# Optimization experiments

Measured on AMD Instinct MI355X. Metric: run time of the kernel, lower is better.

The kernel has to match this reference:

```python
import jax, jax.numpy as jnp
import numpy as np

NEG_SLOPE = 0.2
EPS = 1e-16  # matches PyG softmax epsilon


def gat_conv(x, src, dst, W, att_src, att_dst, bias):
    """PyG-style GATConv (concat heads, self-loops already in src/dst).
    x: [N, F_in]; W: [F_in, H*C]; att_*: [H, C]; bias: [H*C]."""
    N = x.shape[0]
    H, C = att_src.shape
    h = (x @ W).reshape(N, H, C)                       # [N,H,C]
    a_src = jnp.einsum('nhc,hc->nh', h, att_src)       # [N,H]
    a_dst = jnp.einsum('nhc,hc->nh', h, att_dst)
    e = jax.nn.leaky_relu(a_src[src] + a_dst[dst], NEG_SLOPE)   # [E,H]
    # segment softmax over incoming edges of each dst node
    e_max = jax.ops.segment_max(e, dst, num_segments=N)         # [N,H]
    e_max = jnp.where(jnp.isfinite(e_max), e_max, 0.0)
    e_exp = jnp.exp(e - e_max[dst])                              # [E,H]
    denom = jax.ops.segment_sum(e_exp, dst, num_segments=N)     # [N,H]
    alpha = e_exp / (denom[dst] + EPS)                           # [E,H]
    msg = h[src] * alpha[:, :, None]                             # [E,H,C]
    out = jax.ops.segment_sum(msg, dst, num_segments=N)         # [N,H,C]
    return out.reshape(N, H * C) + bias


def setup_inputs() -> dict:
    key = jax.random.key(0)
    ks = jax.random.split(key, 16)
    N, E = 50000, 800000
    F_in, C, H = 1280, 32, 8
    HC = H * C
    NG = 64  # graphs in batch
    x = jax.random.normal(ks[0], (N, F_in), dtype=jnp.float32)
    edge_index = jax.random.randint(ks[1], (2, E), 0, N, dtype=jnp.int64)
    batch = jnp.sort(jax.random.randint(ks[2], (N,), 0, NG, dtype=jnp.int64))
    s = 1.0 / np.sqrt(F_in)
    W1 = jax.random.normal(ks[3], (F_in, HC), dtype=jnp.float32) * s
    as1 = jax.random.normal(ks[4], (H, C), dtype=jnp.float32) * 0.1
    ad1 = jax.random.normal(ks[5], (H, C), dtype=jnp.float32) * 0.1
    b1 = jnp.zeros((HC,), dtype=jnp.float32)
    s2 = 1.0 / np.sqrt(HC)
    W2 = jax.random.normal(ks[6], (HC, HC), dtype=jnp.float32) * s2
    as2 = jax.random.normal(ks[7], (H, C), dtype=jnp.float32) * 0.1
    ad2 = jax.random.normal(ks[8], (H, C), dtype=jnp.float32) * 0.1
    b2 = jnp.zeros((HC,), dtype=jnp.float32)
    lin1_w = jax.random.normal(ks[9], (HC, 128), dtype=jnp.float32) * s2
    lin1_b = jnp.zeros((128,), dtype=jnp.float32)
    lin2_w = jax.random.normal(ks[10], (128, 1), dtype=jnp.float32) * (1.0 / np.sqrt(128))
    lin2_b = jnp.zeros((1,), dtype=jnp.float32)
    return {"x": x, "edge_index": edge_index, "batch": batch,
            "W1": W1, "as1": as1, "ad1": ad1, "b1": b1,
            "W2": W2, "as2": as2, "ad2": ad2, "b2": b2,
            "lin1_w": lin1_w, "lin1_b": lin1_b, "lin2_w": lin2_w, "lin2_b": lin2_b}


def reference(x, edge_index, batch, W1, as1, ad1, b1, W2, as2, ad2, b2,
              lin1_w, lin1_b, lin2_w, lin2_b):
    N = x.shape[0]
    NG = 64
    loops = jnp.arange(N, dtype=edge_index.dtype)
    src = jnp.concatenate([edge_index[0], loops])  # add self-loops (PyG default)
    dst = jnp.concatenate([edge_index[1], loops])
    h = jax.nn.relu(gat_conv(x, src, dst, W1, as1, ad1, b1))
    h = jax.nn.relu(gat_conv(h, src, dst, W2, as2, ad2, b2))
    # global mean pool over graphs
    sums = jax.ops.segment_sum(h, batch, num_segments=NG)               # [NG,HC]
    cnts = jax.ops.segment_sum(jnp.ones((N, 1), h.dtype), batch, num_segments=NG)
    pooled = sums / jnp.maximum(cnts, 1.0)
    z = jax.nn.relu(pooled @ lin1_w + lin1_b)
    out = z @ lin2_w + lin2_b                                            # [NG,1]
    return out.squeeze(-1)
```

## Files before the change

kernel.cpp:

```cpp
#include <hip/hip_runtime.h>
#include <hip/hip_bf16.h>
#include <math.h>

#define HC 256
#define NH 8
#define NEG_SLOPE 0.2f
#define CHW 64
#define LDA 136
#define MR 32

typedef unsigned short u16;
typedef __attribute__((ext_vector_type(8))) short bf16x8;
typedef __attribute__((ext_vector_type(4))) float f32x4;

__device__ __forceinline__ u16 f2bf(float f) {
    unsigned int u = __float_as_uint(f);
    u += 0x7FFFu + ((u >> 16) & 1u);
    return (u16)(u >> 16);
}
__device__ __forceinline__ float bf2f(u16 s) {
    return __uint_as_float(((unsigned int)s) << 16);
}
__device__ __forceinline__ f32x4 bf4f(ushort4 v) {
    f32x4 r;
    r[0] = bf2f(v.x); r[1] = bf2f(v.y); r[2] = bf2f(v.z); r[3] = bf2f(v.w);
    return r;
}

#define BAR_LDS()                                                  \
    do {                                                           \
        asm volatile("s_waitcnt lgkmcnt(0)" ::: "memory");         \
        __builtin_amdgcn_s_barrier();                              \
        __builtin_amdgcn_sched_barrier(0);                         \
    } while (0)

__global__ __launch_bounds__(256) void pack_b_split(const float* __restrict__ B, int K,
                                                    u16* __restrict__ Bh,
                                                    u16* __restrict__ Bl) {
    const int g = blockIdx.x * 256 + threadIdx.x;
    const int lane = g & 63;
    const int f = (g >> 6) & 15;
    const int kt = g >> 10;
    const int col = f * 16 + (lane & 15);
    const int k0 = kt * 32 + (lane >> 4) * 8;
    bf16x8 hv, lv;
#pragma unroll
    for (int e = 0; e < 8; e++) {
        const float v = B[(size_t)(k0 + e) * HC + col];
        const u16 h = f2bf(v);
        hv[e] = (short)h;
        lv[e] = (short)f2bf(v - bf2f(h));
    }
    const size_t off = (size_t)g * 8;
    *(bf16x8*)(Bh + off) = hv;
    *(bf16x8*)(Bl + off) = lv;
}

__global__ __launch_bounds__(256) void gemm_fused_split(
    const float* __restrict__ A,
    const u16* __restrict__ Bh, const u16* __restrict__ Bl,
    float* __restrict__ C, int M, int K) {
    __shared__ u16 ldsA[2][MR * LDA];
    const int tid = threadIdx.x;
    const int wid = tid >> 6;
    const int lane = tid & 63;
    const int rowblk = blockIdx.x;
    const int NG4 = K >> 7;
    const int rot = rowblk % NG4;

    f32x4 acc[2][4];
#pragma unroll
    for (int i = 0; i < 2; i++)
#pragma unroll
        for (int j = 0; j < 4; j++) acc[i][j] = (f32x4)0.f;

    const int srow = tid >> 3;
    const int scc = (tid & 7) * 16;
    const int grow = rowblk * MR + srow;
    const float* aptr = (grow < M) ? (A + (size_t)grow * K + scc) : nullptr;
    const int woff = srow * LDA + scc;

    float4 pf[4];
    auto loadAg = [&](int gg) {
#pragma unroll
        for (int q = 0; q < 4; q++) {
            pf[q] = make_float4(0.f, 0.f, 0.f, 0.f);
            if (aptr) pf[q] = *(const float4*)(aptr + gg * 128 + q * 4);
        }
    };
    auto stageg = [&](int buf) {
#pragma unroll
        for (int p = 0; p < 2; p++) {
            const float vv[8] = {pf[2 * p].x,     pf[2 * p].y,
                                 pf[2 * p].z,     pf[2 * p].w,
                                 pf[2 * p + 1].x, pf[2 * p + 1].y,
                                 pf[2 * p + 1].z, pf[2 * p + 1].w};
            bf16x8 hv;
#pragma unroll
            for (int e = 0; e < 8; e++) hv[e] = (short)f2bf(vv[e]);
            *(bf16x8*)&ldsA[buf][woff + p * 8] = hv;
        }
    };
    auto readA = [&](int buf, int kk, bf16x8* ah) {
#pragma unroll
        for (int i = 0; i < 2; i++)
            ah[i] = *(const bf16x8*)&ldsA[buf][(i * 16 + (lane & 15)) * LDA +
                                              kk * 32 + (lane >> 4) * 8];
    };
    auto loadB = [&](int kt, bf16x8* bh, bf16x8* bl) {
        const u16* bHp = Bh + ((size_t)kt * 16 + wid * 4) * 512 + lane * 8;
        const u16* bLp = Bl + ((size_t)kt * 16 + wid * 4) * 512 + lane * 8;
#pragma unroll
        for (int j = 0; j < 4; j++) {
            bh[j] = *(const bf16x8*)(bHp + j * 512);
            bl[j] = *(const bf16x8*)(bLp + j * 512);
        }
    };
    auto mfma_tile = [&](const bf16x8* ah, const bf16x8* bh, const bf16x8* bl) {
#pragma unroll
        for (int i = 0; i < 2; i++)
#pragma unroll
            for (int j = 0; j < 4; j++) {
                acc[i][j] = __builtin_amdgcn_mfma_f32_16x16x32_bf16(ah[i], bh[j], acc[i][j], 0, 0, 0);
                acc[i][j] = __builtin_amdgcn_mfma_f32_16x16x32_bf16(ah[i], bl[j], acc[i][j], 0, 0, 0);
            }
    };

    loadAg(rot);
    stageg(0);
    if (NG4 > 1) loadAg((rot + 1) % NG4);
    BAR_LDS();

    bf16x8 bh[4], bl[4];

    int cur = 0;
    for (int g = 0; g < NG4; ++g) {
        const int gg = (g + rot) % NG4;
        if (g + 1 < NG4) stageg(cur ^ 1);
        if (g + 2 < NG4) loadAg((g + 2 + rot) % NG4);

        const int kt0 = gg * 4;
#pragma unroll
        for (int kk = 0; kk < 4; kk++) {
            loadB(kt0 + kk, bh, bl);
            bf16x8 ah[2];
            readA(cur, kk, ah);
            mfma_tile(ah, bh, bl);
        }
        BAR_LDS();
        cur ^= 1;
    }

    const int r0 = rowblk * MR;
    const int colb = wid * 64 + (lane & 15);
#pragma unroll
    for (int i = 0; i < 2; i++) {
#pragma unroll
        for (int r = 0; r < 4; r++) {
            const int row = r0 + i * 16 + (lane >> 4) * 4 + r;
            if (row < M) {
#pragma unroll
                for (int j = 0; j < 4; j++)
                    C[(size_t)row * HC + colb + j * 16] = acc[i][j][r];
            }
        }
    }
}

__global__ __launch_bounds__(256) void attn_coef(const float* __restrict__ h,
                                                 const float* __restrict__ att_s,
                                                 const float* __restrict__ att_d,
                                                 float* __restrict__ a_src,
                                                 float* __restrict__ a_dst,
                                                 u16* __restrict__ h_bf) {
    const int n = blockIdx.x;
    const int tid = threadIdx.x;
    const float hv = h[(size_t)n * HC + tid];
    h_bf[(size_t)n * HC + tid] = f2bf(hv);
    float p = hv * att_s[tid];
    float q = hv * att_d[tid];
#pragma unroll
    for (int m = 16; m >= 1; m >>= 1) {
        p += __shfl_xor(p, m);
        q += __shfl_xor(q, m);
    }
    if ((tid & 31) == 0) {
        a_src[n * NH + (tid >> 5)] = p;
        a_dst[n * NH + (tid >> 5)] = q;
    }
}

__global__ void count_deg(const int* __restrict__ dst, int E, int ET, int* __restrict__ deg) {
    const int e = blockIdx.x * blockDim.x + threadIdx.x;
    if (e >= ET) return;
    const int d = (e < E) ? dst[e] : (e - E);
    atomicAdd(&deg[d], 1);
}

__global__ __launch_bounds__(256) void scan_block(const int* __restrict__ deg,
                                                  int* __restrict__ row_ptr,
                                                  int* __restrict__ partials, int N) {
    __shared__ int sd[256];
    const int tid = threadIdx.x;
    const int base = blockIdx.x * 1024 + tid * 4;
    int v0 = (base + 0 < N) ? deg[base + 0] : 0;
    int v1 = (base + 1 < N) ? deg[base + 1] : 0;
    int v2 = (base + 2 < N) ? deg[base + 2] : 0;
    int v3 = (base + 3 < N) ? deg[base + 3] : 0;
    const int tsum = v0 + v1 + v2 + v3;
    sd[tid] = tsum;
    __syncthreads();
    int run = tsum;
    for (int off = 1; off < 256; off <<= 1) {
        int t = 0;
        if (tid >= off) t = sd[tid - off];
        __syncthreads();
        run += t;
        sd[tid] = run;
        __syncthreads();
    }
    const int excl = run - tsum;
    int s0 = excl + v0, s1 = s0 + v1, s2 = s1 + v2, s3 = s2 + v3;
    if (base + 0 < N) row_ptr[base + 1] = s0;
    if (base + 1 < N) row_ptr[base + 2] = s1;
    if (base + 2 < N) row_ptr[base + 3] = s2;
    if (base + 3 < N) row_ptr[base + 4] = s3;
    if (tid == 255) partials[blockIdx.x] = run;
}

__global__ __launch_bounds__(1024) void scan_partials(int* __restrict__ partials, int nb) {
    __shared__ int sd[1024];
    const int tid = threadIdx.x;
    int v = (tid < nb) ? partials[tid] : 0;
    sd[tid] = v;
    __syncthreads();
    int run = v;
    for (int off = 1; off < 1024; off <<= 1) {
        int t = 0;
        if (tid >= off) t = sd[tid - off];
        __syncthreads();
        run += t;
        sd[tid] = run;
        __syncthreads();
    }
    if (tid < nb) partials[tid] = run - v;
}

__global__ __launch_bounds__(256) void scan_add(int* __restrict__ row_ptr,
                                                const int* __restrict__ partials, int N) {
    const int i = blockIdx.x * 256 + threadIdx.x;
    if (i == 0) row_ptr[0] = 0;
    if (i < N) row_ptr[i + 1] += partials[i >> 10];
}

__global__ void scatter_edges(const int* __restrict__ src_in, const int* __restrict__ dst,
                              int E, int ET, const int* __restrict__ row_ptr,
                              int* __restrict__ cursor, int* __restrict__ esrc) {
    const int e = blockIdx.x * blockDim.x + threadIdx.x;
    if (e >= ET) return;
    const int d = (e < E) ? dst[e] : (e - E);
    const int s = (e < E) ? src_in[e] : (e - E);
    const int pos = atomicAdd(&cursor[d], 1);
    esrc[row_ptr[d] + pos] = s;
}

__global__ __launch_bounds__(256) void gat_aggregate_wave(
    const u16* __restrict__ h_bf, const float* __restrict__ a_src,
    const float* __restrict__ a_dst, const int* __restrict__ row_ptr,
    const int* __restrict__ esrc, const float* __restrict__ bias,
    float* __restrict__ out, int N) {
    __shared__ int   s_src[4][CHW];
    __shared__ float s_ev[4][CHW][NH];

    const int tid = threadIdx.x;
    const int wv = tid >> 6;
    const int lane = tid & 63;
    const int n = blockIdx.x * 4 + wv;
    if (n >= N) return;

    const int beg = row_ptr[n];
    const int deg = row_ptr[n + 1] - beg;
    const int jj = lane >> 3;
    const int hh = lane & 7;
    const int g4 = lane >> 3;

    const float adh = a_dst[n * NH + hh];
    float m_run = -1e30f, d_run = 0.f;
    f32x4 acc = (f32x4)0.f;

    for (int c0 = 0; c0 < deg; c0 += CHW) {
        const int chlen = min(CHW, deg - c0);

        float lmax = -1e30f;
        for (int p = 0; p < chlen; p += 8) {
            const int j = p + jj;
            if (j < chlen) {
                const int s = esrc[beg + c0 + j];
                if (hh == 0) s_src[wv][j] = s;
                float v = a_src[s * NH + hh] + adh;
                v = (v > 0.f) ? v : NEG_SLOPE * v;
                s_ev[wv][j][hh] = v;
                lmax = fmaxf(lmax, v);
            }
        }
        lmax = fmaxf(lmax, __shfl_xor(lmax, 8));
        lmax = fmaxf(lmax, __shfl_xor(lmax, 16));
        lmax = fmaxf(lmax, __shfl_xor(lmax, 32));
        const float mo = m_run;
        const float mn = fmaxf(mo, lmax);
        const float scl = __expf(mo - mn);
        m_run = mn;

        float lsum = 0.f;
        for (int p = 0; p < chlen; p += 8) {
            const int j = p + jj;
            if (j < chlen) {
                const float pv = __expf(s_ev[wv][j][hh] - mn);
                s_ev[wv][j][hh] = pv;
                lsum += pv;
            }
        }
        lsum += __shfl_xor(lsum, 8);
        lsum += __shfl_xor(lsum, 16);
        lsum += __shfl_xor(lsum, 32);
        d_run = d_run * scl + lsum;

        __asm__ volatile("s_waitcnt lgkmcnt(0)" ::: "memory");

        const float scl4 = __shfl(scl, g4);
        f32x4 t0 = (f32x4)0.f, t1 = (f32x4)0.f, t2 = (f32x4)0.f, t3 = (f32x4)0.f;
        int j = 0;
        for (; j + 4 <= chlen; j += 4) {
            const int s0 = s_src[wv][j],     s1 = s_src[wv][j + 1];
            const int s2 = s_src[wv][j + 2], s3 = s_src[wv][j + 3];
            const float p0 = s_ev[wv][j][g4],     p1 = s_ev[wv][j + 1][g4];
            const float p2 = s_ev[wv][j + 2][g4], p3 = s_ev[wv][j + 3][g4];
            const f32x4 h0 = bf4f(*(const ushort4*)&h_bf[(size_t)s0 * HC + lane * 4]);
            const f32x4 h1 = bf4f(*(const ushort4*)&h_bf[(size_t)s1 * HC + lane * 4]);
            const f32x4 h2 = bf4f(*(const ushort4*)&h_bf[(size_t)s2 * HC + lane * 4]);
            const f32x4 h3 = bf4f(*(const ushort4*)&h_bf[(size_t)s3 * HC + lane * 4]);
#pragma unroll
            for (int q = 0; q < 4; q++) {
                t0[q] += p0 * h0[q];
                t1[q] += p1 * h1[q];
                t2[q] += p2 * h2[q];
                t3[q] += p3 * h3[q];
            }
        }
        for (; j < chlen; j++) {
            const int s0 = s_src[wv][j];
            const float p0 = s_ev[wv][j][g4];
            const f32x4 h0 = bf4f(*(const ushort4*)&h_bf[(size_t)s0 * HC + lane * 4]);
#pragma unroll
            for (int q = 0; q < 4; q++) t0[q] += p0 * h0[q];
        }
#pragma unroll
        for (int q = 0; q < 4; q++)
            acc[q] = acc[q] * scl4 + ((t0[q] + t1[q]) + (t2[q] + t3[q]));
    }

    const float invd = 1.f / (__shfl(d_run, g4) + 1e-16f);
    const f32x4 bv = *(const f32x4*)&bias[lane * 4];
    f32x4 o;
#pragma unroll
    for (int q = 0; q < 4; q++) o[q] = fmaxf(acc[q] * invd + bv[q], 0.f);
    *(f32x4*)&out[(size_t)n * HC + lane * 4] = o;
}

__global__ __launch_bounds__(256) void pool_partial(const float* __restrict__ h,
                                                    const int* __restrict__ batch, int N,
                                                    float* __restrict__ sums) {
    __shared__ int bs[64];
    const int tid = threadIdx.x;
    const int base = blockIdx.x * 64;
    const int cnt = min(64, N - base);
    if (tid < 64 && tid < cnt) bs[tid] = batch[base + tid];
    __syncthreads();

    float acc = 0.f;
    int cur = bs[0];
    for (int i = 0; i < cnt; i++) {
        const int g = bs[i];
        if (g != cur) {
            atomicAdd(&sums[(size_t)cur * HC + tid], acc);
            acc = 0.f;
            cur = g;
        }
        acc += h[(size_t)(base + i) * HC + tid];
    }
    atomicAdd(&sums[(size_t)cur * HC + tid], acc);
}

__global__ __launch_bounds__(256) void pool_div(float* __restrict__ sums,
                                                const int* __restrict__ batch, int N) {
    const int g = blockIdx.x;
    const int tid = threadIdx.x;
    int lo = 0, hi = N;
    while (lo < hi) {
        const int mid = (lo + hi) >> 1;
        if (batch[mid] < g) lo = mid + 1; else hi = mid;
    }
    const int start = lo;
    hi = N;
    while (lo < hi) {
        const int mid = (lo + hi) >> 1;
        if (batch[mid] < g + 1) lo = mid + 1; else hi = mid;
    }
    const float inv = 1.f / fmaxf((float)(lo - start), 1.0f);
    sums[(size_t)g * HC + tid] *= inv;
}

__global__ __launch_bounds__(128) void mlp_head(const float* __restrict__ pooled,
                                                const float* __restrict__ w1,
                                                const float* __restrict__ b1,
                                                const float* __restrict__ w2,
                                                const float* __restrict__ b2,
                                                float* __restrict__ out) {
    const int g = blockIdx.x;
    const int tid = threadIdx.x;
    __shared__ float p[HC];
    p[tid] = pooled[g * HC + tid];
    p[tid + 128] = pooled[g * HC + tid + 128];
    __syncthreads();
    float z = b1[tid];
#pragma unroll 8
    for (int k = 0; k < HC; k++) z += p[k] * w1[k * 128 + tid];
    z = fmaxf(z, 0.f);
    float t = z * w2[tid];
#pragma unroll
    for (int m = 32; m >= 1; m >>= 1) t += __shfl_xor(t, m);
    __shared__ float ws2[2];
    if ((tid & 63) == 0) ws2[tid >> 6] = t;
    __syncthreads();
    if (tid == 0) out[g] = ws2[0] + ws2[1] + b2[0];
}

extern "C" void kernel_launch(void* const* d_in, const int* in_sizes, int n_in,
                              void* d_out, int out_size, void* d_ws, size_t ws_size,
                              hipStream_t stream) {
    const float* x      = (const float*)d_in[0];
    const int*   ei     = (const int*)d_in[1];
    const int*   batch  = (const int*)d_in[2];
    const float* W1     = (const float*)d_in[3];
    const float* as1    = (const float*)d_in[4];
    const float* ad1    = (const float*)d_in[5];
    const float* b1     = (const float*)d_in[6];
    const float* W2     = (const float*)d_in[7];
    const float* as2    = (const float*)d_in[8];
    const float* ad2    = (const float*)d_in[9];
    const float* b2     = (const float*)d_in[10];
    const float* lin1w  = (const float*)d_in[11];
    const float* lin1b  = (const float*)d_in[12];
    const float* lin2w  = (const float*)d_in[13];
    const float* lin2b  = (const float*)d_in[14];

    const int N   = in_sizes[2];
    const int E   = in_sizes[1] / 2;
    const int ET  = E + N;
    const int Fin = in_sizes[0] / N;
    const int NG  = 64;

    const int nRB = (N + MR - 1) / MR;
    const int nScanBlk = (N + 1023) / 1024;

    const int* src_arr = ei;
    const int* dst_arr = ei + E;

    char* ws = (char*)d_ws;
    size_t off = 0;
    auto alloc = [&](size_t bytes) {
        void* p = ws + off;
        off += (bytes + 255) & ~(size_t)255;
        return p;
    };
    float* h_gemm  = (float*)alloc((size_t)N * HC * sizeof(float));
    float* h_agg   = (float*)alloc((size_t)N * HC * sizeof(float));
    u16*   h_bf    = (u16*)alloc((size_t)N * HC * sizeof(u16));
    float* a_src   = (float*)alloc((size_t)N * NH * sizeof(float));
    float* a_dst   = (float*)alloc((size_t)N * NH * sizeof(float));
    int*   deg     = (int*)alloc((size_t)N * sizeof(int));
    int*   cursor  = (int*)alloc((size_t)N * sizeof(int));
    int*   row_ptr = (int*)alloc((size_t)(N + 1) * sizeof(int));
    int*   partials= (int*)alloc((size_t)1024 * sizeof(int));
    int*   esrc    = (int*)alloc((size_t)ET * sizeof(int));
    float* pooled  = (float*)alloc((size_t)NG * HC * sizeof(float));
    u16* Bh = (u16*)alloc((size_t)Fin * HC * sizeof(u16));
    u16* Bl = (u16*)alloc((size_t)Fin * HC * sizeof(u16));
    (void)ws_size; (void)n_in; (void)out_size;

    hipMemsetAsync(deg, 0, (size_t)N * sizeof(int), stream);
    hipMemsetAsync(cursor, 0, (size_t)N * sizeof(int), stream);
    {
        const int blocks = (ET + 255) / 256;
        count_deg<<<blocks, 256, 0, stream>>>(dst_arr, E, ET, deg);
        scan_block<<<nScanBlk, 256, 0, stream>>>(deg, row_ptr, partials, N);
        scan_partials<<<1, 1024, 0, stream>>>(partials, nScanBlk);
        scan_add<<<(N + 255) / 256, 256, 0, stream>>>(row_ptr, partials, N);
        scatter_edges<<<blocks, 256, 0, stream>>>(src_arr, dst_arr, E, ET, row_ptr,
                                                  cursor, esrc);
    }

    const int aggBlocks = (N + 3) / 4;

    pack_b_split<<<(Fin / 32) * 4, 256, 0, stream>>>(W1, Fin, Bh, Bl);
    gemm_fused_split<<<nRB, 256, 0, stream>>>(x, Bh, Bl, h_gemm, N, Fin);
    attn_coef<<<N, 256, 0, stream>>>(h_gemm, as1, ad1, a_src, a_dst, h_bf);
    gat_aggregate_wave<<<aggBlocks, 256, 0, stream>>>(h_bf, a_src, a_dst, row_ptr,
                                                      esrc, b1, h_agg, N);

    pack_b_split<<<(HC / 32) * 4, 256, 0, stream>>>(W2, HC, Bh, Bl);
    gemm_fused_split<<<nRB, 256, 0, stream>>>(h_agg, Bh, Bl, h_gemm, N, HC);
    attn_coef<<<N, 256, 0, stream>>>(h_gemm, as2, ad2, a_src, a_dst, h_bf);
    gat_aggregate_wave<<<aggBlocks, 256, 0, stream>>>(h_bf, a_src, a_dst, row_ptr,
                                                      esrc, b2, h_agg, N);

    hipMemsetAsync(pooled, 0, (size_t)NG * HC * sizeof(float), stream);
    pool_partial<<<(N + 63) / 64, 256, 0, stream>>>(h_agg, batch, N, pooled);
    pool_div<<<NG, 256, 0, stream>>>(pooled, batch, N);
    mlp_head<<<NG, 128, 0, stream>>>(pooled, lin1w, lin1b, lin2w, lin2b, (float*)d_out);
}
```

Before: 521.6 us.

## Fuse attention coefficients into GEMM epilogue and pass bf16 activations between layers

The attn_coef kernel is removed. The GEMM epilogue now computes per-head a_src/a_dst dot products with shuffles and writes the bf16 projected features directly, so no fp32 h buffer is written and re-read. The first aggregation writes bf16 output, which the second GEMM loads without conversion. This saves two launches and several N×256 fp32 round trips. It also changes where bf16 rounding of the layer-1 output happens, which was already rounded to bf16 inside the GEMM before.

```diff
diff --git a/kernel.cpp b/kernel.cpp
--- a/kernel.cpp
+++ b/kernel.cpp
@@ -56,10 +56,13 @@
     *(bf16x8*)(Bl + off) = lv;
 }
 
-__global__ __launch_bounds__(256) void gemm_fused_split(
-    const float* __restrict__ A,
+template <typename AT>
+__global__ __launch_bounds__(256) void gemm_fused(
+    const AT* __restrict__ A,
     const u16* __restrict__ Bh, const u16* __restrict__ Bl,
-    float* __restrict__ C, int M, int K) {
+    const float* __restrict__ att_s, const float* __restrict__ att_d,
+    u16* __restrict__ h_out, float* __restrict__ a_src, float* __restrict__ a_dst,
+    int M, int K) {
     __shared__ u16 ldsA[2][MR * LDA];
     const int tid = threadIdx.x;
     const int wid = tid >> 6;
@@ -77,28 +80,43 @@
     const int srow = tid >> 3;
     const int scc = (tid & 7) * 16;
     const int grow = rowblk * MR + srow;
-    const float* aptr = (grow < M) ? (A + (size_t)grow * K + scc) : nullptr;
+    const AT* aptr = (grow < M) ? (A + (size_t)grow * K + scc) : nullptr;
     const int woff = srow * LDA + scc;
 
     float4 pf[4];
+    uint4 pu[2];
     auto loadAg = [&](int gg) {
-#pragma unroll
-        for (int q = 0; q < 4; q++) {
-            pf[q] = make_float4(0.f, 0.f, 0.f, 0.f);
-            if (aptr) pf[q] = *(const float4*)(aptr + gg * 128 + q * 4);
+        if constexpr (sizeof(AT) == 4) {
+#pragma unroll
+            for (int q = 0; q < 4; q++) {
+                pf[q] = make_float4(0.f, 0.f, 0.f, 0.f);
+                if (aptr) pf[q] = *(const float4*)((const float*)aptr + gg * 128 + q * 4);
+            }
+        } else {
+            pu[0] = make_uint4(0, 0, 0, 0);
+            pu[1] = make_uint4(0, 0, 0, 0);
+            if (aptr) {
+                pu[0] = *(const uint4*)((const u16*)aptr + gg * 128);
+                pu[1] = *(const uint4*)((const u16*)aptr + gg * 128 + 8);
+            }
         }
     };
     auto stageg = [&](int buf) {
-#pragma unroll
-        for (int p = 0; p < 2; p++) {
-            const float vv[8] = {pf[2 * p].x,     pf[2 * p].y,
-                                 pf[2 * p].z,     pf[2 * p].w,
-                                 pf[2 * p + 1].x, pf[2 * p + 1].y,
-                                 pf[2 * p + 1].z, pf[2 * p + 1].w};
-            bf16x8 hv;
-#pragma unroll
-            for (int e = 0; e < 8; e++) hv[e] = (short)f2bf(vv[e]);
-            *(bf16x8*)&ldsA[buf][woff + p * 8] = hv;
+        if constexpr (sizeof(AT) == 4) {
+#pragma unroll
+            for (int p = 0; p < 2; p++) {
+                const float vv[8] = {pf[2 * p].x,     pf[2 * p].y,
+                                     pf[2 * p].z,     pf[2 * p].w,
+                                     pf[2 * p + 1].x, pf[2 * p + 1].y,
+                                     pf[2 * p + 1].z, pf[2 * p + 1].w};
+                bf16x8 hv;
+#pragma unroll
+                for (int e = 0; e < 8; e++) hv[e] = (short)f2bf(vv[e]);
+                *(bf16x8*)&ldsA[buf][woff + p * 8] = hv;
+            }
+        } else {
+            *(uint4*)&ldsA[buf][woff] = pu[0];
+            *(uint4*)&ldsA[buf][woff + 8] = pu[1];
         }
     };
     auto readA = [&](int buf, int kk, bf16x8* ah) {
@@ -132,7 +150,6 @@
     BAR_LDS();
 
     bf16x8 bh[4], bl[4];
-
     int cur = 0;
     for (int g = 0; g < NG4; ++g) {
         const int gg = (g + rot) % NG4;
@@ -153,40 +170,40 @@
 
     const int r0 = rowblk * MR;
     const int colb = wid * 64 + (lane & 15);
+    float asw[4], adw[4];
+#pragma unroll
+    for (int j = 0; j < 4; j++) {
+        asw[j] = att_s[colb + j * 16];
+        adw[j] = att_d[colb + j * 16];
+    }
 #pragma unroll
     for (int i = 0; i < 2; i++) {
 #pragma unroll
         for (int r = 0; r < 4; r++) {
             const int row = r0 + i * 16 + (lane >> 4) * 4 + r;
+            float ps0 = acc[i][0][r] * asw[0] + acc[i][1][r] * asw[1];
+            float ps1 = acc[i][2][r] * asw[2] + acc[i][3][r] * asw[3];
+            float pd0 = acc[i][0][r] * adw[0] + acc[i][1][r] * adw[1];
+            float pd1 = acc[i][2][r] * adw[2] + acc[i][3][r] * adw[3];
+#pragma unroll
+            for (int m = 1; m <= 8; m <<= 1) {
+                ps0 += __shfl_xor(ps0, m);
+                ps1 += __shfl_xor(ps1, m);
+                pd0 += __shfl_xor(pd0, m);
+                pd1 += __shfl_xor(pd1, m);
+            }
             if (row < M) {
 #pragma unroll
                 for (int j = 0; j < 4; j++)
-                    C[(size_t)row * HC + colb + j * 16] = acc[i][j][r];
-            }
-        }
-    }
-}
-
-__global__ __launch_bounds__(256) void attn_coef(const float* __restrict__ h,
-                                                 const float* __restrict__ att_s,
-                                                 const float* __restrict__ att_d,
-                                                 float* __restrict__ a_src,
-                                                 float* __restrict__ a_dst,
-                                                 u16* __restrict__ h_bf) {
-    const int n = blockIdx.x;
-    const int tid = threadIdx.x;
-    const float hv = h[(size_t)n * HC + tid];
-    h_bf[(size_t)n * HC + tid] = f2bf(hv);
-    float p = hv * att_s[tid];
-    float q = hv * att_d[tid];
-#pragma unroll
-    for (int m = 16; m >= 1; m >>= 1) {
-        p += __shfl_xor(p, m);
-        q += __shfl_xor(q, m);
-    }
-    if ((tid & 31) == 0) {
-        a_src[n * NH + (tid >> 5)] = p;
-        a_dst[n * NH + (tid >> 5)] = q;
+                    h_out[(size_t)row * HC + colb + j * 16] = f2bf(acc[i][j][r]);
+                if ((lane & 15) == 0) {
+                    a_src[row * NH + 2 * wid + 0] = ps0;
+                    a_src[row * NH + 2 * wid + 1] = ps1;
+                    a_dst[row * NH + 2 * wid + 0] = pd0;
+                    a_dst[row * NH + 2 * wid + 1] = pd1;
+                }
+            }
+        }
     }
 }
 
@@ -264,11 +281,12 @@
     esrc[row_ptr[d] + pos] = s;
 }
 
+template <typename OT>
 __global__ __launch_bounds__(256) void gat_aggregate_wave(
     const u16* __restrict__ h_bf, const float* __restrict__ a_src,
     const float* __restrict__ a_dst, const int* __restrict__ row_ptr,
     const int* __restrict__ esrc, const float* __restrict__ bias,
-    float* __restrict__ out, int N) {
+    OT* __restrict__ out, int N) {
     __shared__ int   s_src[4][CHW];
     __shared__ float s_ev[4][CHW][NH];
 
@@ -361,10 +379,19 @@
 
     const float invd = 1.f / (__shfl(d_run, g4) + 1e-16f);
     const f32x4 bv = *(const f32x4*)&bias[lane * 4];
-    f32x4 o;
-#pragma unroll
-    for (int q = 0; q < 4; q++) o[q] = fmaxf(acc[q] * invd + bv[q], 0.f);
-    *(f32x4*)&out[(size_t)n * HC + lane * 4] = o;
+    if constexpr (sizeof(OT) == 2) {
+        ushort4 o4;
+        o4.x = f2bf(fmaxf(acc[0] * invd + bv[0], 0.f));
+        o4.y = f2bf(fmaxf(acc[1] * invd + bv[1], 0.f));
+        o4.z = f2bf(fmaxf(acc[2] * invd + bv[2], 0.f));
+        o4.w = f2bf(fmaxf(acc[3] * invd + bv[3], 0.f));
+        *(ushort4*)&out[(size_t)n * HC + lane * 4] = o4;
+    } else {
+        f32x4 o;
+#pragma unroll
+        for (int q = 0; q < 4; q++) o[q] = fmaxf(acc[q] * invd + bv[q], 0.f);
+        *(f32x4*)&out[(size_t)n * HC + lane * 4] = o;
+    }
 }
 
 __global__ __launch_bounds__(256) void pool_partial(const float* __restrict__ h,
@@ -473,9 +500,9 @@
         off += (bytes + 255) & ~(size_t)255;
         return p;
     };
-    float* h_gemm  = (float*)alloc((size_t)N * HC * sizeof(float));
     float* h_agg   = (float*)alloc((size_t)N * HC * sizeof(float));
-    u16*   h_bf    = (u16*)alloc((size_t)N * HC * sizeof(u16));
+    u16*   hb_a    = (u16*)alloc((size_t)N * HC * sizeof(u16));
+    u16*   hb_b    = (u16*)alloc((size_t)N * HC * sizeof(u16));
     float* a_src   = (float*)alloc((size_t)N * NH * sizeof(float));
     float* a_dst   = (float*)alloc((size_t)N * NH * sizeof(float));
     int*   deg     = (int*)alloc((size_t)N * sizeof(int));
@@ -503,16 +530,16 @@
     const int aggBlocks = (N + 3) / 4;
 
     pack_b_split<<<(Fin / 32) * 4, 256, 0, stream>>>(W1, Fin, Bh, Bl);
-    gemm_fused_split<<<nRB, 256, 0, stream>>>(x, Bh, Bl, h_gemm, N, Fin);
-    attn_coef<<<N, 256, 0, stream>>>(h_gemm, as1, ad1, a_src, a_dst, h_bf);
-    gat_aggregate_wave<<<aggBlocks, 256, 0, stream>>>(h_bf, a_src, a_dst, row_ptr,
-                                                      esrc, b1, h_agg, N);
+    gemm_fused<float><<<nRB, 256, 0, stream>>>(x, Bh, Bl, as1, ad1,
+                                               hb_a, a_src, a_dst, N, Fin);
+    gat_aggregate_wave<u16><<<aggBlocks, 256, 0, stream>>>(hb_a, a_src, a_dst, row_ptr,
+                                                           esrc, b1, hb_b, N);
 
     pack_b_split<<<(HC / 32) * 4, 256, 0, stream>>>(W2, HC, Bh, Bl);
-    gemm_fused_split<<<nRB, 256, 0, stream>>>(h_agg, Bh, Bl, h_gemm, N, HC);
-    attn_coef<<<N, 256, 0, stream>>>(h_gemm, as2, ad2, a_src, a_dst, h_bf);
-    gat_aggregate_wave<<<aggBlocks, 256, 0, stream>>>(h_bf, a_src, a_dst, row_ptr,
-                                                      esrc, b2, h_agg, N);
+    gemm_fused<u16><<<nRB, 256, 0, stream>>>(hb_b, Bh, Bl, as2, ad2,
+                                             hb_a, a_src, a_dst, N, HC);
+    gat_aggregate_wave<float><<<aggBlocks, 256, 0, stream>>>(hb_a, a_src, a_dst, row_ptr,
+                                                             esrc, b2, h_agg, N);
 
     hipMemsetAsync(pooled, 0, (size_t)NG * HC * sizeof(float), stream);
     pool_partial<<<(N + 63) / 64, 256, 0, stream>>>(h_agg, batch, N, pooled);
```

Measured after the change: 468.5 us. 1.11x faster.
